# Kernel optimization log

Hardware: AMD Instinct MI355X
Metric: run time of the kernel (lower is better)

Reference implementation:

```python
import jax, jax.numpy as jnp
import numpy as np


def setup_inputs() -> dict:
    key = jax.random.key(0)
    k1, k2 = jax.random.split(key)
    shape = (32, 1024, 1024)
    x = jax.random.normal(k1, shape, dtype=jnp.float32)
    y = jax.random.normal(k2, shape, dtype=jnp.float32)
    return {"x": x, "y": y}


def reference(x, y):
    # Loss1.forward: mean of |y - x| over positions where x > y.
    # Since x > y there, |y - x| == x - y.
    xf = x.reshape(-1)
    yf = y.reshape(-1)
    mask = xf > yf
    loss_sum = jnp.sum(jnp.where(mask, xf - yf, 0.0))
    count = jnp.sum(mask).astype(xf.dtype)
    # original returns 0 when count == 0
    return jnp.where(count > 0, loss_sum / jnp.maximum(count, 1.0), 0.0)
```

## Files before the change

kernel.cpp:

```cpp
#include <hip/hip_runtime.h>

#define NBLOCKS 2048
#define NTHREADS 256
#define TILE_V4 (NTHREADS * 4)

typedef float vf4 __attribute__((ext_vector_type(4)));

__device__ __forceinline__ void stage16(const vf4* g, vf4* l) {
    __builtin_amdgcn_global_load_lds(
        (const __attribute__((address_space(1))) void*)g,
        (__attribute__((address_space(3))) void*)l,
        16, 0, 0);
}

__global__ __launch_bounds__(NTHREADS) void loss1_partial(
    const float* __restrict__ x, const float* __restrict__ y,
    long long n, float* __restrict__ psum, int* __restrict__ pcnt) {
    const long long nvec = n >> 2;
    const long long ntiles = nvec / TILE_V4;
    const vf4* __restrict__ x4 = (const vf4*)x;
    const vf4* __restrict__ y4 = (const vf4*)y;

    __shared__ vf4 ybuf[TILE_V4];

    float s = 0.0f;
    int c = 0;

    for (long long t = blockIdx.x; t < ntiles; t += gridDim.x) {
        long long p = t * TILE_V4 + threadIdx.x;

        #pragma unroll
        for (int u = 0; u < 4; ++u)
            stage16(&y4[p + u * NTHREADS], &ybuf[threadIdx.x + u * NTHREADS]);

        vf4 a0 = __builtin_nontemporal_load(&x4[p]);
        vf4 a1 = __builtin_nontemporal_load(&x4[p + NTHREADS]);
        vf4 a2 = __builtin_nontemporal_load(&x4[p + 2 * NTHREADS]);
        vf4 a3 = __builtin_nontemporal_load(&x4[p + 3 * NTHREADS]);

        __syncthreads();

        vf4 b0 = ybuf[threadIdx.x];
        vf4 b1 = ybuf[threadIdx.x + NTHREADS];
        vf4 b2 = ybuf[threadIdx.x + 2 * NTHREADS];
        vf4 b3 = ybuf[threadIdx.x + 3 * NTHREADS];

        #pragma unroll
        for (int k = 0; k < 4; ++k) {
            s += (a0[k] > b0[k]) ? (a0[k] - b0[k]) : 0.0f;  c += (a0[k] > b0[k]);
            s += (a1[k] > b1[k]) ? (a1[k] - b1[k]) : 0.0f;  c += (a1[k] > b1[k]);
            s += (a2[k] > b2[k]) ? (a2[k] - b2[k]) : 0.0f;  c += (a2[k] > b2[k]);
            s += (a3[k] > b3[k]) ? (a3[k] - b3[k]) : 0.0f;  c += (a3[k] > b3[k]);
        }

        __syncthreads();
    }

    {
        long long gtid = (long long)blockIdx.x * blockDim.x + threadIdx.x;
        long long gstride = (long long)gridDim.x * blockDim.x;
        for (long long i = ntiles * TILE_V4 + gtid; i < nvec; i += gstride) {
            vf4 a = x4[i];
            vf4 b = y4[i];
            #pragma unroll
            for (int k = 0; k < 4; ++k) {
                s += (a[k] > b[k]) ? (a[k] - b[k]) : 0.0f;  c += (a[k] > b[k]);
            }
        }
        if (gtid == 0) {
            for (long long j = nvec << 2; j < n; ++j) {
                float d = x[j] - y[j];
                if (x[j] > y[j]) { s += d; c += 1; }
            }
        }
    }

    #pragma unroll
    for (int off = 32; off > 0; off >>= 1) {
        s += __shfl_down(s, off, 64);
        c += __shfl_down(c, off, 64);
    }

    __shared__ float ss[NTHREADS / 64];
    __shared__ int   sc[NTHREADS / 64];
    int lane = threadIdx.x & 63;
    int wave = threadIdx.x >> 6;
    if (lane == 0) { ss[wave] = s; sc[wave] = c; }
    __syncthreads();
    if (threadIdx.x == 0) {
        float ts = 0.0f; int tc = 0;
        #pragma unroll
        for (int w = 0; w < NTHREADS / 64; ++w) { ts += ss[w]; tc += sc[w]; }
        psum[blockIdx.x] = ts;
        pcnt[blockIdx.x] = tc;
    }
}

__global__ __launch_bounds__(1024) void loss1_final(
    const float* __restrict__ psum, const int* __restrict__ pcnt,
    int nparts, float* __restrict__ out) {
    int tid = threadIdx.x;
    float s = 0.0f;
    int c = 0;
    for (int i = tid; i < nparts; i += 1024) {
        s += psum[i];
        c += pcnt[i];
    }
    #pragma unroll
    for (int off = 32; off > 0; off >>= 1) {
        s += __shfl_down(s, off, 64);
        c += __shfl_down(c, off, 64);
    }
    __shared__ float ss[16];
    __shared__ int   sc[16];
    int lane = tid & 63;
    int wave = tid >> 6;
    if (lane == 0) { ss[wave] = s; sc[wave] = c; }
    __syncthreads();
    if (tid == 0) {
        float ts = 0.0f; int tc = 0;
        #pragma unroll
        for (int w = 0; w < 16; ++w) { ts += ss[w]; tc += sc[w]; }
        out[0] = (tc > 0) ? (ts / (float)tc) : 0.0f;
    }
}

extern "C" void kernel_launch(void* const* d_in, const int* in_sizes, int n_in,
                              void* d_out, int out_size, void* d_ws, size_t ws_size,
                              hipStream_t stream) {
    const float* x = (const float*)d_in[0];
    const float* y = (const float*)d_in[1];
    long long n = (long long)in_sizes[0];

    float* psum = (float*)d_ws;
    int*   pcnt = (int*)((char*)d_ws + NBLOCKS * sizeof(float));

    loss1_partial<<<NBLOCKS, NTHREADS, 0, stream>>>(x, y, n, psum, pcnt);
    loss1_final<<<1, 1024, 0, stream>>>(psum, pcnt, NBLOCKS, (float*)d_out);
}
```

Measured before the change: 261.6 us.

## Double-buffer LDS staging to prefetch next tile while computing current

Restructures the streaming loop into a software pipeline: y for the next tile is staged into a second LDS buffer and the next x vectors are loaded into registers while the current tile is reduced. Explicit vmcnt waits and raw barriers replace __syncthreads. It also halves the grid to 1024 blocks and counts mask hits with ballot/popcount, using fmax in place of a select. This hides memory latency per block at the cost of more registers and LDS, and the hand-written waitcnt values are fragile.

```diff
diff --git a/kernel.cpp b/kernel.cpp
--- a/kernel.cpp
+++ b/kernel.cpp
@@ -1,6 +1,6 @@
 #include <hip/hip_runtime.h>
 
-#define NBLOCKS 2048
+#define NBLOCKS 1024
 #define NTHREADS 256
 #define TILE_V4 (NTHREADS * 4)
 
@@ -21,39 +21,84 @@
     const vf4* __restrict__ x4 = (const vf4*)x;
     const vf4* __restrict__ y4 = (const vf4*)y;
 
-    __shared__ vf4 ybuf[TILE_V4];
+    __shared__ vf4 ybuf[2][TILE_V4];
 
-    float s = 0.0f;
-    int c = 0;
+    float s  = 0.0f;
+    int   cw = 0;
+    int   ct = 0;
 
-    for (long long t = blockIdx.x; t < ntiles; t += gridDim.x) {
+    long long t = blockIdx.x;
+    bool have = (t < ntiles);
+    vf4 a0, a1, a2, a3;
+
+    if (have) {
         long long p = t * TILE_V4 + threadIdx.x;
-
         #pragma unroll
         for (int u = 0; u < 4; ++u)
-            stage16(&y4[p + u * NTHREADS], &ybuf[threadIdx.x + u * NTHREADS]);
+            stage16(&y4[p + u * NTHREADS], &ybuf[0][threadIdx.x + u * NTHREADS]);
+        a0 = __builtin_nontemporal_load(&x4[p]);
+        a1 = __builtin_nontemporal_load(&x4[p + NTHREADS]);
+        a2 = __builtin_nontemporal_load(&x4[p + 2 * NTHREADS]);
+        a3 = __builtin_nontemporal_load(&x4[p + 3 * NTHREADS]);
+    }
 
-        vf4 a0 = __builtin_nontemporal_load(&x4[p]);
-        vf4 a1 = __builtin_nontemporal_load(&x4[p + NTHREADS]);
-        vf4 a2 = __builtin_nontemporal_load(&x4[p + 2 * NTHREADS]);
-        vf4 a3 = __builtin_nontemporal_load(&x4[p + 3 * NTHREADS]);
+    int cur = 0;
+    while (have) {
+        const long long tn = t + gridDim.x;
+        const bool haven = (tn < ntiles);
 
-        __syncthreads();
+        vf4 na0, na1, na2, na3;
+        if (haven) {
+            long long pn = tn * TILE_V4 + threadIdx.x;
+            #pragma unroll
+            for (int u = 0; u < 4; ++u)
+                stage16(&y4[pn + u * NTHREADS],
+                        &ybuf[cur ^ 1][threadIdx.x + u * NTHREADS]);
+            na0 = __builtin_nontemporal_load(&x4[pn]);
+            na1 = __builtin_nontemporal_load(&x4[pn + NTHREADS]);
+            na2 = __builtin_nontemporal_load(&x4[pn + 2 * NTHREADS]);
+            na3 = __builtin_nontemporal_load(&x4[pn + 3 * NTHREADS]);
+        }
 
-        vf4 b0 = ybuf[threadIdx.x];
-        vf4 b1 = ybuf[threadIdx.x + NTHREADS];
-        vf4 b2 = ybuf[threadIdx.x + 2 * NTHREADS];
-        vf4 b3 = ybuf[threadIdx.x + 3 * NTHREADS];
+        if (haven) {
+            asm volatile("s_waitcnt vmcnt(8)" ::: "memory");
+        } else {
+            asm volatile("s_waitcnt vmcnt(0)" ::: "memory");
+        }
+        __builtin_amdgcn_sched_barrier(0);
+        __builtin_amdgcn_s_barrier();
+        __builtin_amdgcn_sched_barrier(0);
+
+        vf4 b0 = ybuf[cur][threadIdx.x];
+        vf4 b1 = ybuf[cur][threadIdx.x + NTHREADS];
+        vf4 b2 = ybuf[cur][threadIdx.x + 2 * NTHREADS];
+        vf4 b3 = ybuf[cur][threadIdx.x + 3 * NTHREADS];
 
         #pragma unroll
         for (int k = 0; k < 4; ++k) {
-            s += (a0[k] > b0[k]) ? (a0[k] - b0[k]) : 0.0f;  c += (a0[k] > b0[k]);
-            s += (a1[k] > b1[k]) ? (a1[k] - b1[k]) : 0.0f;  c += (a1[k] > b1[k]);
-            s += (a2[k] > b2[k]) ? (a2[k] - b2[k]) : 0.0f;  c += (a2[k] > b2[k]);
-            s += (a3[k] > b3[k]) ? (a3[k] - b3[k]) : 0.0f;  c += (a3[k] > b3[k]);
+            float d0 = a0[k] - b0[k];
+            float d1 = a1[k] - b1[k];
+            float d2 = a2[k] - b2[k];
+            float d3 = a3[k] - b3[k];
+            s += fmaxf(d0, 0.0f);
+            s += fmaxf(d1, 0.0f);
+            s += fmaxf(d2, 0.0f);
+            s += fmaxf(d3, 0.0f);
+            cw += (int)__popcll(__ballot(a0[k] > b0[k]));
+            cw += (int)__popcll(__ballot(a1[k] > b1[k]));
+            cw += (int)__popcll(__ballot(a2[k] > b2[k]));
+            cw += (int)__popcll(__ballot(a3[k] > b3[k]));
         }
 
-        __syncthreads();
+        asm volatile("s_waitcnt lgkmcnt(0)" ::: "memory");
+        __builtin_amdgcn_sched_barrier(0);
+        __builtin_amdgcn_s_barrier();
+        __builtin_amdgcn_sched_barrier(0);
+
+        if (haven) { a0 = na0; a1 = na1; a2 = na2; a3 = na3; }
+        cur ^= 1;
+        t = tn;
+        have = haven;
     }
 
     {
@@ -64,28 +109,28 @@
             vf4 b = y4[i];
             #pragma unroll
             for (int k = 0; k < 4; ++k) {
-                s += (a[k] > b[k]) ? (a[k] - b[k]) : 0.0f;  c += (a[k] > b[k]);
+                s += (a[k] > b[k]) ? (a[k] - b[k]) : 0.0f;  ct += (a[k] > b[k]);
             }
         }
         if (gtid == 0) {
             for (long long j = nvec << 2; j < n; ++j) {
                 float d = x[j] - y[j];
-                if (x[j] > y[j]) { s += d; c += 1; }
+                if (x[j] > y[j]) { s += d; ct += 1; }
             }
         }
     }
 
     #pragma unroll
     for (int off = 32; off > 0; off >>= 1) {
-        s += __shfl_down(s, off, 64);
-        c += __shfl_down(c, off, 64);
+        s  += __shfl_down(s, off, 64);
+        ct += __shfl_down(ct, off, 64);
     }
 
     __shared__ float ss[NTHREADS / 64];
     __shared__ int   sc[NTHREADS / 64];
     int lane = threadIdx.x & 63;
     int wave = threadIdx.x >> 6;
-    if (lane == 0) { ss[wave] = s; sc[wave] = c; }
+    if (lane == 0) { ss[wave] = s; sc[wave] = ct + cw; }
     __syncthreads();
     if (threadIdx.x == 0) {
         float ts = 0.0f; int tc = 0;
```

Result: no change. 262.1 us (+0.2%).

## Replace LDS-staged y loads with direct register loads and wave-ballot counting

Applied to the files above, without the earlier changes.

Removes the global_load_lds staging of y into shared memory and the two per-tile barriers, so x and y are now both loaded straight into registers with ordinary (no longer nontemporal) loads. The masked difference becomes fmaxf(x-y,0), and the count is computed per wave with ballot plus popcount instead of per-lane increments. Occupancy is hinted through a launch-bounds minimum of 8 blocks. The goal is to cut barrier stalls and LDS traffic in a bandwidth-bound reduction, at the cost of losing the nontemporal cache hint and the async LDS path.

```diff
diff --git a/kernel.cpp b/kernel.cpp
--- a/kernel.cpp
+++ b/kernel.cpp
@@ -6,14 +6,7 @@
 
 typedef float vf4 __attribute__((ext_vector_type(4)));
 
-__device__ __forceinline__ void stage16(const vf4* g, vf4* l) {
-    __builtin_amdgcn_global_load_lds(
-        (const __attribute__((address_space(1))) void*)g,
-        (__attribute__((address_space(3))) void*)l,
-        16, 0, 0);
-}
-
-__global__ __launch_bounds__(NTHREADS) void loss1_partial(
+__global__ __launch_bounds__(NTHREADS, 8) void loss1_partial(
     const float* __restrict__ x, const float* __restrict__ y,
     long long n, float* __restrict__ psum, int* __restrict__ pcnt) {
     const long long nvec = n >> 2;
@@ -21,39 +14,33 @@
     const vf4* __restrict__ x4 = (const vf4*)x;
     const vf4* __restrict__ y4 = (const vf4*)y;
 
-    __shared__ vf4 ybuf[TILE_V4];
-
-    float s = 0.0f;
-    int c = 0;
+    float s  = 0.0f;
+    int   cw = 0;
+    int   ct = 0;
 
     for (long long t = blockIdx.x; t < ntiles; t += gridDim.x) {
         long long p = t * TILE_V4 + threadIdx.x;
 
-        #pragma unroll
-        for (int u = 0; u < 4; ++u)
-            stage16(&y4[p + u * NTHREADS], &ybuf[threadIdx.x + u * NTHREADS]);
-
-        vf4 a0 = __builtin_nontemporal_load(&x4[p]);
-        vf4 a1 = __builtin_nontemporal_load(&x4[p + NTHREADS]);
-        vf4 a2 = __builtin_nontemporal_load(&x4[p + 2 * NTHREADS]);
-        vf4 a3 = __builtin_nontemporal_load(&x4[p + 3 * NTHREADS]);
-
-        __syncthreads();
-
-        vf4 b0 = ybuf[threadIdx.x];
-        vf4 b1 = ybuf[threadIdx.x + NTHREADS];
-        vf4 b2 = ybuf[threadIdx.x + 2 * NTHREADS];
-        vf4 b3 = ybuf[threadIdx.x + 3 * NTHREADS];
+        vf4 a0 = x4[p];
+        vf4 a1 = x4[p + NTHREADS];
+        vf4 a2 = x4[p + 2 * NTHREADS];
+        vf4 a3 = x4[p + 3 * NTHREADS];
+        vf4 b0 = y4[p];
+        vf4 b1 = y4[p + NTHREADS];
+        vf4 b2 = y4[p + 2 * NTHREADS];
+        vf4 b3 = y4[p + 3 * NTHREADS];
 
         #pragma unroll
         for (int k = 0; k < 4; ++k) {
-            s += (a0[k] > b0[k]) ? (a0[k] - b0[k]) : 0.0f;  c += (a0[k] > b0[k]);
-            s += (a1[k] > b1[k]) ? (a1[k] - b1[k]) : 0.0f;  c += (a1[k] > b1[k]);
-            s += (a2[k] > b2[k]) ? (a2[k] - b2[k]) : 0.0f;  c += (a2[k] > b2[k]);
-            s += (a3[k] > b3[k]) ? (a3[k] - b3[k]) : 0.0f;  c += (a3[k] > b3[k]);
+            s += fmaxf(a0[k] - b0[k], 0.0f);
+            s += fmaxf(a1[k] - b1[k], 0.0f);
+            s += fmaxf(a2[k] - b2[k], 0.0f);
+            s += fmaxf(a3[k] - b3[k], 0.0f);
+            cw += (int)__popcll(__ballot(a0[k] > b0[k]));
+            cw += (int)__popcll(__ballot(a1[k] > b1[k]));
+            cw += (int)__popcll(__ballot(a2[k] > b2[k]));
+            cw += (int)__popcll(__ballot(a3[k] > b3[k]));
         }
-
-        __syncthreads();
     }
 
     {
@@ -64,28 +51,28 @@
             vf4 b = y4[i];
             #pragma unroll
             for (int k = 0; k < 4; ++k) {
-                s += (a[k] > b[k]) ? (a[k] - b[k]) : 0.0f;  c += (a[k] > b[k]);
+                s += (a[k] > b[k]) ? (a[k] - b[k]) : 0.0f;  ct += (a[k] > b[k]);
             }
         }
         if (gtid == 0) {
             for (long long j = nvec << 2; j < n; ++j) {
                 float d = x[j] - y[j];
-                if (x[j] > y[j]) { s += d; c += 1; }
+                if (x[j] > y[j]) { s += d; ct += 1; }
             }
         }
     }
 
     #pragma unroll
     for (int off = 32; off > 0; off >>= 1) {
-        s += __shfl_down(s, off, 64);
-        c += __shfl_down(c, off, 64);
+        s  += __shfl_down(s, off, 64);
+        ct += __shfl_down(ct, off, 64);
     }
 
     __shared__ float ss[NTHREADS / 64];
     __shared__ int   sc[NTHREADS / 64];
     int lane = threadIdx.x & 63;
     int wave = threadIdx.x >> 6;
-    if (lane == 0) { ss[wave] = s; sc[wave] = c; }
+    if (lane == 0) { ss[wave] = s; sc[wave] = ct + cw; }
     __syncthreads();
     if (threadIdx.x == 0) {
         float ts = 0.0f; int tc = 0;
```

After: 271.6 us. 1.04x slower.
